# Performance work log

Measured on AMD Instinct MI355X. Metric: run time of the kernel, lower is better.

Reference implementation:

```python
import jax, jax.numpy as jnp
import numpy as np

NUM_LAYERS = 4
HID = 512
EMB = 512
VOCAB = 50000
SOU_LEN = 256
TAR_LEN = 50
BATCH = 8
VEXT = VOCAB + SOU_LEN


def _gru_layer(x, h0, wih, whh, bih, bhh):
    # x: [B,T,in], h0: [B,H]; PyTorch GRU gate order: r, z, n
    def step(h, xt):
        gi = xt @ wih.T + bih
        gh = h @ whh.T + bhh
        ir, iz, inn = jnp.split(gi, 3, axis=-1)
        hr, hz, hn = jnp.split(gh, 3, axis=-1)
        r = jax.nn.sigmoid(ir + hr)
        z = jax.nn.sigmoid(iz + hz)
        n = jnp.tanh(inn + r * hn)
        h_new = (1.0 - z) * n + z * h
        return h_new, h_new
    _, ys = jax.lax.scan(step, h0, jnp.swapaxes(x, 0, 1))
    return jnp.swapaxes(ys, 0, 1)


def _forward(sou, tar, hidden, encoder_outputs, extended_length,
             emb, gru_wih, gru_whh, gru_bih, gru_bhh,
             fc_enc_w, fc_enc_b, fc_dec_w, fc_dec_b, v_w,
             fc_out1_w, fc_out1_b, fc_out2_w, fc_out2_b,
             g1_w, g1_b, g2_w, g2_b, g3_w, g3_b):
    emb = emb.at[0].set(0.0)  # padding_idx=0 (also zeroes its grad)
    tar_emb = emb[tar]  # [B,T,E]
    # pack_padded_sequence: only first `length` steps processed, rest padded with 0
    lengths = jnp.maximum(jnp.sum(tar > 0, axis=-1), 1)
    x = tar_emb
    for l in range(gru_wih.shape[0]):
        x = _gru_layer(x, hidden[l], gru_wih[l], gru_whh[l], gru_bih[l], gru_bhh[l])
    t_idx = jnp.arange(x.shape[1])
    dec_out = jnp.where((t_idx[None, :] < lengths[:, None])[:, :, None], x, 0.0)  # [B,T,H]
    # additive (Bahdanau) attention
    e1 = encoder_outputs @ fc_enc_w.T + fc_enc_b          # [B,S,H]
    e2 = dec_out @ fc_dec_w.T + fc_dec_b                  # [B,T,H]
    energy = jnp.tanh(e1[:, None, :, :] + e2[:, :, None, :])  # [B,T,S,H]
    scores = jnp.einsum('btsh,h->bts', energy, v_w)
    scores = jnp.where((sou == 0)[:, None, :], -jnp.inf, scores)
    atten = jax.nn.softmax(scores, axis=-1)               # [B,T,S]
    weighted = jnp.einsum('bts,bsh->bth', atten, encoder_outputs)
    all_out = jnp.concatenate([weighted, dec_out], axis=-1)  # [B,T,2H]
    mid = all_out @ fc_out2_w.T + fc_out2_b
    logits = mid @ fc_out1_w.T + fc_out1_b                # [B,T,VEXT]
    # extended-vocab mask (vectorized version of the per-batch python loop)
    col = jnp.arange(logits.shape[-1])
    valid = col[None, None, :] < (VOCAB + extended_length)[:, None, None]
    logits = jnp.where(valid, logits, -1e9)
    output_gen = jax.nn.softmax(logits, axis=-1)
    # copy mechanism: scatter-add attention into extended vocab (replaces sparse one-hot bmm)
    def _scatter(att_b, sou_b):
        return jnp.zeros((att_b.shape[0], VEXT), att_b.dtype).at[:, sou_b].add(att_b)
    output_copy = jax.vmap(_scatter)(atten, sou)          # [B,T,VEXT]
    gate = jax.nn.sigmoid(
        jnp.einsum('bth,h->bt', weighted, g1_w) + g1_b[0]
        + jnp.einsum('bth,h->bt', dec_out, g2_w) + g2_b[0]
        + jnp.einsum('bte,e->bt', tar_emb, g3_w) + g3_b[0])[:, :, None]
    output = (1.0 - gate) * output_gen + gate * output_copy
    return output, atten


def setup_inputs() -> dict:
    key = jax.random.key(0)
    ks = jax.random.split(key, 24)
    s = 0.02
    return {
        'sou': jax.random.randint(ks[0], (BATCH, SOU_LEN), 0, VEXT),
        'tar': jax.random.randint(ks[1], (BATCH, TAR_LEN), 0, VEXT),
        'hidden': jax.random.normal(ks[2], (NUM_LAYERS, BATCH, HID), jnp.float32),
        'encoder_outputs': jax.random.normal(ks[3], (BATCH, SOU_LEN, HID), jnp.float32),
        'extended_length': jax.random.randint(ks[4], (BATCH,), 0, SOU_LEN),
        'emb': jax.random.normal(ks[5], (VEXT, EMB), jnp.float32) * s,
        'gru_wih': jax.random.normal(ks[6], (NUM_LAYERS, 3 * HID, EMB), jnp.float32) * s,
        'gru_whh': jax.random.normal(ks[7], (NUM_LAYERS, 3 * HID, HID), jnp.float32) * s,
        'gru_bih': jax.random.normal(ks[8], (NUM_LAYERS, 3 * HID), jnp.float32) * s,
        'gru_bhh': jax.random.normal(ks[9], (NUM_LAYERS, 3 * HID), jnp.float32) * s,
        'fc_enc_w': jax.random.normal(ks[10], (HID, HID), jnp.float32) * s,
        'fc_enc_b': jax.random.normal(ks[11], (HID,), jnp.float32) * s,
        'fc_dec_w': jax.random.normal(ks[12], (HID, HID), jnp.float32) * s,
        'fc_dec_b': jax.random.normal(ks[13], (HID,), jnp.float32) * s,
        'v_w': jax.random.normal(ks[14], (HID,), jnp.float32) * s,
        'fc_out1_w': jax.random.normal(ks[15], (VEXT, HID), jnp.float32) * s,
        'fc_out1_b': jax.random.normal(ks[16], (VEXT,), jnp.float32) * s,
        'fc_out2_w': jax.random.normal(ks[17], (HID, 2 * HID), jnp.float32) * s,
        'fc_out2_b': jax.random.normal(ks[18], (HID,), jnp.float32) * s,
        'g1_w': jax.random.normal(ks[19], (HID,), jnp.float32) * s,
        'g1_b': jnp.zeros((1,), jnp.float32),
        'g2_w': jax.random.normal(ks[20], (HID,), jnp.float32) * s,
        'g2_b': jnp.zeros((1,), jnp.float32),
        'g3_w': jax.random.normal(ks[21], (EMB,), jnp.float32) * s,
        'g3_b': jnp.zeros((1,), jnp.float32),
    }


def reference(sou, tar, hidden, encoder_outputs, extended_length,
              emb, gru_wih, gru_whh, gru_bih, gru_bhh,
              fc_enc_w, fc_enc_b, fc_dec_w, fc_dec_b, v_w,
              fc_out1_w, fc_out1_b, fc_out2_w, fc_out2_b,
              g1_w, g1_b, g2_w, g2_b, g3_w, g3_b):
    return _forward(sou, tar, hidden, encoder_outputs, extended_length,
                    emb, gru_wih, gru_whh, gru_bih, gru_bhh,
                    fc_enc_w, fc_enc_b, fc_dec_w, fc_dec_b, v_w,
                    fc_out1_w, fc_out1_b, fc_out2_w, fc_out2_b,
                    g1_w, g1_b, g2_w, g2_b, g3_w, g3_b)
```

## Files before the change

kernel.cpp:

```cpp
#include <hip/hip_runtime.h>

typedef unsigned short u16;
typedef unsigned int u32;

using bf16x8 = __attribute__((ext_vector_type(8))) short;
using f32x4  = __attribute__((ext_vector_type(4))) float;

#define VOCAB 50000
#define VEXT  50256
#define OUT_AT_OFF 20102400L

__device__ __forceinline__ u16 f2b(float f) {
  u32 x = __float_as_uint(f);
  u32 r = (x + 0x7fffu + ((x >> 16) & 1u)) >> 16;
  return (u16)r;
}

__device__ __forceinline__ u32 sload(const u32* p) {
  return __hip_atomic_load(p, __ATOMIC_RELAXED, __HIP_MEMORY_SCOPE_SYSTEM);
}
__device__ __forceinline__ void sstore(u32* p, u32 v) {
  __hip_atomic_store(p, v, __ATOMIC_RELAXED, __HIP_MEMORY_SCOPE_SYSTEM);
}
__device__ __forceinline__ bf16x8 sload8(const u32* p) {
  union { u32 u[4]; bf16x8 v; } x;
  x.u[0] = sload(p); x.u[1] = sload(p + 1);
  x.u[2] = sload(p + 2); x.u[3] = sload(p + 3);
  return x.v;
}

__global__ void k_conv(const float* __restrict__ src, u16* __restrict__ dst,
                       long realN, long totalN) {
  long i = (long)blockIdx.x * 256 + threadIdx.x;
  if (i >= totalN) return;
  float v = (i < realN) ? src[i] : 0.f;
  dst[i] = f2b(v);
}

__global__ void k_h0b(const float* __restrict__ hidden, u16* __restrict__ h0B) {
  int i = blockIdx.x * 256 + threadIdx.x;
  int l = i >> 13, rem = i & 8191, rr = rem >> 9, k = rem & 511;
  float v = (rr < 8) ? hidden[((long)l * 8 + rr) * 512 + k] : 0.f;
  h0B[i] = f2b(v);
}

__global__ __launch_bounds__(256) void k_prep(const int* __restrict__ tar,
                                              const float* __restrict__ emb,
                                              const float* __restrict__ g3w,
                                              u16* __restrict__ xB0,
                                              float* __restrict__ g3dot) {
  int r = blockIdx.x;
  int tid = threadIdx.x;
  int idx = tar[r];
  __shared__ float red[256];
  float p = 0.f;
  for (int k = tid; k < 512; k += 256) {
    float v = (idx == 0) ? 0.f : emb[(long)idx * 512 + k];
    xB0[(long)r * 512 + k] = f2b(v);
    p += v * g3w[k];
  }
  red[tid] = p; __syncthreads();
  for (int o = 128; o > 0; o >>= 1) { if (tid < o) red[tid] += red[tid + o]; __syncthreads(); }
  if (tid == 0) g3dot[r] = red[0];
}

__global__ void k_lengths(const int* __restrict__ tar, int* __restrict__ lens) {
  int b = threadIdx.x;
  if (b < 8) {
    int c = 0;
    for (int t = 0; t < 50; t++) c += (tar[b * 50 + t] > 0) ? 1 : 0;
    lens[b] = (c > 0) ? c : 1;
  }
}

__global__ __launch_bounds__(256) void k_mask(float* __restrict__ x4f,
                                              const int* __restrict__ lens) {
  int r = blockIdx.x, b = r / 50, t = r % 50;
  if (t >= lens[b])
    for (int k = threadIdx.x; k < 512; k += 256) x4f[(long)r * 512 + k] = 0.f;
}

__device__ __forceinline__ void wait_flags(const u32* f, u32 target) {
  const int lane = threadIdx.x & 63;
  const u32* p = f + (lane & 31) * 16;
  unsigned it = 0;
  while (true) {
    u32 v = sload(p);
    if (__all((int)(v >= target))) break;
    __builtin_amdgcn_s_sleep(2);
    if (++it > (1u << 20)) break;
  }
  asm volatile("" ::: "memory");
}

__global__ __launch_bounds__(128, 1) void k_gru(
    const u16* __restrict__ wihB, const u16* __restrict__ whhB,
    const float* __restrict__ bih, const float* __restrict__ bhh,
    const float* __restrict__ hidden, const u16* __restrict__ h0B,
    u16* __restrict__ xB,
    u32* __restrict__ hX,
    float* __restrict__ x4f,
    u32* __restrict__ flags)
{
  const int wg = blockIdx.x;
  const int l = wg >> 5;
  const int wg32 = wg & 31;
  const int c0 = wg32 << 4;
  const int tid = threadIdx.x;
  const int wv = tid >> 6;
  const int lane = tid & 63;
  const int lrow = lane & 15;
  const int q = lane >> 4;

  __shared__ float giX[2][3][16][16];

  const u16* Wsrc = (wv == 0 ? wihB : whhB) + (long)l * 1536 * 512;

  const int col = c0 + lrow;
  const float bir = bih[l * 1536 + col],         bhr = bhh[l * 1536 + col];
  const float biz = bih[l * 1536 + 512 + col],   bhz = bhh[l * 1536 + 512 + col];
  const float bin_ = bih[l * 1536 + 1024 + col], bhn = bhh[l * 1536 + 1024 + col];

  const u16* xin = xB + (long)l * 16 * 50 * 512;
  u32* xBu = (u32*)xB;
  u32* x4u = (u32*)x4f;

  float hreg[4];
  if (wv == 1) {
#pragma unroll
    for (int rg = 0; rg < 4; rg++) {
      int bb = q * 4 + rg;
      hreg[rg] = (bb < 8) ? hidden[((long)l * 8 + bb) * 512 + col] : 0.f;
    }
  }

  for (int t = 0; t < 50; t++) {
    bf16x8 af[16];
    if (wv == 0) {
      if (l > 0) {
        wait_flags(flags + (l - 1) * 512, (u32)(t + 1));
        const u32* As32 = (const u32*)xin + (long)lrow * 50 * 256 + (long)t * 256;
#pragma unroll
        for (int ks = 0; ks < 16; ks++) af[ks] = sload8(As32 + ks * 16 + q * 4);
      } else {
        const u16* Asrc = xin + (long)lrow * 50 * 512 + (long)t * 512;
#pragma unroll
        for (int ks = 0; ks < 16; ks++) af[ks] = *(const bf16x8*)(Asrc + ks * 32 + q * 8);
      }
    } else {
      if (t > 0) {
        wait_flags(flags + l * 512, (u32)t);
        const u32* Hs = hX + (((long)l * 2 + ((t - 1) & 1)) * 16 + lrow) * 256;
#pragma unroll
        for (int ks = 0; ks < 16; ks++) af[ks] = sload8(Hs + ks * 16 + q * 4);
      } else {
        const u16* Asrc = h0B + ((long)l * 16 + lrow) * 512;
#pragma unroll
        for (int ks = 0; ks < 16; ks++) af[ks] = *(const bf16x8*)(Asrc + ks * 32 + q * 8);
      }
    }

    f32x4 a0 = {0.f, 0.f, 0.f, 0.f}, a1 = {0.f, 0.f, 0.f, 0.f}, a2 = {0.f, 0.f, 0.f, 0.f};
#pragma unroll
    for (int ks = 0; ks < 16; ks++) {
      bf16x8 b0 = *(const bf16x8*)(Wsrc + (long)(0 * 512 + c0 + lrow) * 512 + ks * 32 + q * 8);
      bf16x8 b1 = *(const bf16x8*)(Wsrc + (long)(1 * 512 + c0 + lrow) * 512 + ks * 32 + q * 8);
      bf16x8 b2 = *(const bf16x8*)(Wsrc + (long)(2 * 512 + c0 + lrow) * 512 + ks * 32 + q * 8);
      a0 = __builtin_amdgcn_mfma_f32_16x16x32_bf16(af[ks], b0, a0, 0, 0, 0);
      a1 = __builtin_amdgcn_mfma_f32_16x16x32_bf16(af[ks], b1, a1, 0, 0, 0);
      a2 = __builtin_amdgcn_mfma_f32_16x16x32_bf16(af[ks], b2, a2, 0, 0, 0);
    }

    if (wv == 0) {
#pragma unroll
      for (int rg = 0; rg < 4; rg++) {
        giX[t & 1][0][q * 4 + rg][lrow] = a0[rg];
        giX[t & 1][1][q * 4 + rg][lrow] = a1[rg];
        giX[t & 1][2][q * 4 + rg][lrow] = a2[rg];
      }
    }
    __syncthreads();

    if (wv == 1) {
#pragma unroll
      for (int rg = 0; rg < 4; rg++) {
        int bb = q * 4 + rg;
        float hnew = 0.f;
        u16 hb16 = 0;
        if (bb < 8) {
          float gir = giX[t & 1][0][bb][lrow] + bir;
          float giz = giX[t & 1][1][bb][lrow] + biz;
          float gin = giX[t & 1][2][bb][lrow] + bin_;
          float ghr = a0[rg] + bhr;
          float ghz = a1[rg] + bhz;
          float ghn = a2[rg] + bhn;
          float hprev = hreg[rg];
          float rr = 1.f / (1.f + expf(-(gir + ghr)));
          float zz = 1.f / (1.f + expf(-(giz + ghz)));
          float nn = tanhf(gin + rr * ghn);
          hnew = (1.f - zz) * nn + zz * hprev;
          hreg[rg] = hnew;
          hb16 = f2b(hnew);
        }
        int other = __shfl_xor((int)hb16, 1);
        if (bb < 8) {
          if ((lane & 1) == 0) {
            u32 pr = (u32)hb16 | ((u32)(u16)other << 16);
            long slot = ((long)l * 2 + (t & 1)) * 16 + bb;
            sstore(hX + slot * 256 + (col >> 1), pr);
            if (l < 3)
              sstore(xBu + (((long)(l + 1) * 16 + bb) * 50 + t) * 256 + (col >> 1), pr);
          }
          if (l == 3)
            sstore(x4u + ((long)bb * 50 + t) * 512 + col, __float_as_uint(hnew));
        }
      }
      if (lane == 0)
        __hip_atomic_store(flags + ((long)l * 32 + wg32) * 16, (u32)(t + 1),
                           __ATOMIC_RELEASE, __HIP_MEMORY_SCOPE_SYSTEM);
    }
  }
}

__global__ __launch_bounds__(256, 2) void k_gemm_bf16(
    const u16* __restrict__ A, const u16* __restrict__ Bm,
    const float* __restrict__ bias, float* __restrict__ C,
    int M, int N, int K, int ldc)
{
  __shared__ __align__(16) u16 As[4096];
  __shared__ __align__(16) u16 Bs[4096];
  const int tid = threadIdx.x;
  const int wv = tid >> 6, lane = tid & 63;
  const int wm = wv >> 1, wn = wv & 1;
  const int lrow = lane & 15, q = lane >> 4;
  const int m0 = blockIdx.y * 128, n0 = blockIdx.x * 128;

  f32x4 acc[4][4];
#pragma unroll
  for (int i = 0; i < 4; i++)
#pragma unroll
    for (int j = 0; j < 4; j++) acc[i][j] = {0.f, 0.f, 0.f, 0.f};

  for (int k0 = 0; k0 < K; k0 += 32) {
#pragma unroll
    for (int i = 0; i < 2; i++) {
      int c = i * 256 + tid;
      int row = c >> 2, ko = (c & 3) << 3;
      *(uint4*)(As + c * 8) = *(const uint4*)(A + (long)(m0 + row) * K + k0 + ko);
      *(uint4*)(Bs + c * 8) = *(const uint4*)(Bm + (long)(n0 + row) * K + k0 + ko);
    }
    __syncthreads();
    bf16x8 af[4], bfr[4];
#pragma unroll
    for (int i = 0; i < 4; i++) af[i] = *(const bf16x8*)(As + (wm * 64 + i * 16 + lrow) * 32 + q * 8);
#pragma unroll
    for (int j = 0; j < 4; j++) bfr[j] = *(const bf16x8*)(Bs + (wn * 64 + j * 16 + lrow) * 32 + q * 8);
#pragma unroll
    for (int i = 0; i < 4; i++)
#pragma unroll
      for (int j = 0; j < 4; j++)
        acc[i][j] = __builtin_amdgcn_mfma_f32_16x16x32_bf16(af[i], bfr[j], acc[i][j], 0, 0, 0);
    __syncthreads();
  }

#pragma unroll
  for (int i = 0; i < 4; i++) {
    int rbase = m0 + wm * 64 + i * 16 + q * 4;
#pragma unroll
    for (int j = 0; j < 4; j++) {
      int colg = n0 + wn * 64 + j * 16 + lrow;
      if (colg < N) {
        float bv = bias[colg];
#pragma unroll
        for (int rg = 0; rg < 4; rg++) {
          int rowg = rbase + rg;
          if (rowg < M) C[(long)rowg * ldc + colg] = acc[i][j][rg] + bv;
        }
      }
    }
  }
}

__global__ __launch_bounds__(256) void k_attn(
    const float* __restrict__ e1, const float* __restrict__ e2,
    const float* __restrict__ enc, const float* __restrict__ x4f,
    const int* __restrict__ sou, const float* __restrict__ vw,
    const float* __restrict__ g1w, const float* __restrict__ g1b,
    const float* __restrict__ g2w, const float* __restrict__ g2b,
    const float* __restrict__ g3b, const float* __restrict__ g3dot,
    float* __restrict__ all_out, float* __restrict__ gate,
    float* __restrict__ atten_out)
{
  int r = blockIdx.x;
  int b = r / 50;
  int tid = threadIdx.x;
  __shared__ float e2s[512], decs[512], at[256], red[256];
  for (int k = tid; k < 512; k += 256) {
    e2s[k] = e2[(long)r * 512 + k];
    decs[k] = x4f[(long)r * 512 + k];
  }
  __syncthreads();
  const float* erow = e1 + ((long)b * 256 + tid) * 512;
  float sc = 0.f;
#pragma unroll 4
  for (int h = 0; h < 512; h++) sc += vw[h] * tanhf(erow[h] + e2s[h]);
  if (sou[b * 256 + tid] == 0) sc = -INFINITY;

  red[tid] = sc; __syncthreads();
  for (int o = 128; o > 0; o >>= 1) { if (tid < o) red[tid] = fmaxf(red[tid], red[tid + o]); __syncthreads(); }
  float mx = red[0]; __syncthreads();
  float p = expf(sc - mx);
  red[tid] = p; __syncthreads();
  for (int o = 128; o > 0; o >>= 1) { if (tid < o) red[tid] += red[tid + o]; __syncthreads(); }
  float S = red[0]; __syncthreads();
  float a = p / S;
  at[tid] = a;
  atten_out[(long)r * 256 + tid] = a;
  __syncthreads();

  float pg = 0.f;
  for (int h = tid; h < 512; h += 256) {
    float wsum = 0.f;
    const float* ecol = enc + (long)b * 256 * 512 + h;
    for (int s = 0; s < 256; s++) wsum += at[s] * ecol[(long)s * 512];
    all_out[(long)r * 1024 + h] = wsum;
    all_out[(long)r * 1024 + 512 + h] = decs[h];
    pg += wsum * g1w[h] + decs[h] * g2w[h];
  }
  red[tid] = pg; __syncthreads();
  for (int o = 128; o > 0; o >>= 1) { if (tid < o) red[tid] += red[tid + o]; __syncthreads(); }
  if (tid == 0) {
    float z = red[0] + g1b[0] + g2b[0] + g3dot[r] + g3b[0];
    gate[r] = 1.f / (1.f + expf(-z));
  }
}

__global__ __launch_bounds__(1024) void k_softmax(float* __restrict__ out,
                                                  const float* __restrict__ gate,
                                                  const int* __restrict__ ext) {
  int r = blockIdx.x;
  int b = r / 50;
  int tid = threadIdx.x;
  int nv = VOCAB + ext[b];
  __shared__ float red[1024];
  float* row = out + (long)r * VEXT;
  float m = -INFINITY;
  for (int c = tid; c < nv; c += 1024) m = fmaxf(m, row[c]);
  red[tid] = m; __syncthreads();
  for (int o = 512; o > 0; o >>= 1) { if (tid < o) red[tid] = fmaxf(red[tid], red[tid + o]); __syncthreads(); }
  m = red[0]; __syncthreads();
  float s = 0.f;
  for (int c = tid; c < nv; c += 1024) s += expf(row[c] - m);
  red[tid] = s; __syncthreads();
  for (int o = 512; o > 0; o >>= 1) { if (tid < o) red[tid] += red[tid + o]; __syncthreads(); }
  float inv = (1.f - gate[r]) / red[0];
  for (int c = tid; c < VEXT; c += 1024) {
    float v = (c < nv) ? expf(row[c] - m) * inv : 0.f;
    row[c] = v;
  }
}

__global__ void k_scatter(float* __restrict__ out, const float* __restrict__ atten,
                          const float* __restrict__ gate, const int* __restrict__ sou) {
  int r = blockIdx.x, s = threadIdx.x;
  int b = r / 50;
  float v = gate[r] * atten[(long)r * 256 + s];
  int colv = sou[b * 256 + s];
  atomicAdd(out + (long)r * VEXT + colv, v);
}

extern "C" void kernel_launch(void* const* d_in, const int* in_sizes, int n_in,
                              void* d_out, int out_size, void* d_ws, size_t ws_size,
                              hipStream_t stream) {
  (void)in_sizes; (void)n_in; (void)out_size;
  const int* sou = (const int*)d_in[0];
  const int* tar = (const int*)d_in[1];
  const float* hidden = (const float*)d_in[2];
  const float* enc = (const float*)d_in[3];
  const int* ext = (const int*)d_in[4];
  const float* emb = (const float*)d_in[5];
  const float* wih = (const float*)d_in[6];
  const float* whh = (const float*)d_in[7];
  const float* bih = (const float*)d_in[8];
  const float* bhh = (const float*)d_in[9];
  const float* fc_enc_w = (const float*)d_in[10];
  const float* fc_enc_b = (const float*)d_in[11];
  const float* fc_dec_w = (const float*)d_in[12];
  const float* fc_dec_b = (const float*)d_in[13];
  const float* v_w = (const float*)d_in[14];
  const float* w1 = (const float*)d_in[15];
  const float* b1 = (const float*)d_in[16];
  const float* w2 = (const float*)d_in[17];
  const float* b2 = (const float*)d_in[18];
  const float* g1w = (const float*)d_in[19];
  const float* g1b = (const float*)d_in[20];
  const float* g2w = (const float*)d_in[21];
  const float* g2b = (const float*)d_in[22];
  const float* g3w = (const float*)d_in[23];
  const float* g3b = (const float*)d_in[24];
  float* out = (float*)d_out;

  char* base = (char*)d_ws;
  size_t cur = 0;
  auto alloc = [&](size_t bytes) -> void* {
    void* r = base + cur;
    cur = (cur + bytes + 255) & ~(size_t)255;
    return r;
  };
  u16* wihB = (u16*)alloc(6291456);
  u16* whhB = (u16*)alloc(6291456);
  u16* w1B  = (u16*)alloc(51511296);
  u16* encB = (u16*)alloc(2097152);
  u16* fceB = (u16*)alloc(524288);
  u16* fcdB = (u16*)alloc(524288);
  u16* fo2B = (u16*)alloc(1048576);
  u16* midB = (u16*)alloc(524288);
  u16* decB = (u16*)alloc(524288);
  u16* allB = (u16*)alloc(1048576);
  u16* xB   = (u16*)alloc(3276800);
  u16* h0B  = (u16*)alloc(65536);
  u32* hX   = (u32*)alloc(131072);
  float* x4f = (float*)alloc(819200);
  float* e1 = (float*)alloc(4194304);
  float* e2 = (float*)alloc(819200);
  float* allo = (float*)alloc(1638400);
  float* mid = (float*)alloc(819200);
  float* g3dot = (float*)alloc(1600);
  float* gate = (float*)alloc(1600);
  int* lens = (int*)alloc(32);
  u32* flags = (u32*)alloc(8192);
  if (cur > ws_size) return;

  hipMemsetAsync(flags, 0, 8192, stream);

  k_conv<<<12288, 256, 0, stream>>>(wih, wihB, 3145728L, 3145728L);
  k_conv<<<12288, 256, 0, stream>>>(whh, whhB, 3145728L, 3145728L);
  k_conv<<<100608, 256, 0, stream>>>(w1, w1B, 25731072L, 25755648L);
  k_conv<<<4096, 256, 0, stream>>>(enc, encB, 1048576L, 1048576L);
  k_conv<<<1024, 256, 0, stream>>>(fc_enc_w, fceB, 262144L, 262144L);
  k_conv<<<1024, 256, 0, stream>>>(fc_dec_w, fcdB, 262144L, 262144L);
  k_conv<<<2048, 256, 0, stream>>>(w2, fo2B, 524288L, 524288L);
  k_h0b<<<128, 256, 0, stream>>>(hidden, h0B);
  k_prep<<<400, 256, 0, stream>>>(tar, emb, g3w, xB, g3dot);
  k_lengths<<<1, 64, 0, stream>>>(tar, lens);

  k_gru<<<128, 128, 0, stream>>>(wihB, whhB, bih, bhh, hidden, h0B, xB, hX, x4f, flags);
  k_mask<<<400, 256, 0, stream>>>(x4f, lens);
  k_conv<<<1024, 256, 0, stream>>>(x4f, decB, 204800L, 262144L);

  k_gemm_bf16<<<dim3(4, 16), 256, 0, stream>>>(encB, fceB, fc_enc_b, e1, 2048, 512, 512, 512);
  k_gemm_bf16<<<dim3(4, 4), 256, 0, stream>>>(decB, fcdB, fc_dec_b, e2, 400, 512, 512, 512);
  k_attn<<<400, 256, 0, stream>>>(e1, e2, enc, x4f, sou, v_w, g1w, g1b, g2w, g2b, g3b,
                                  g3dot, allo, gate, out + OUT_AT_OFF);
  k_conv<<<2048, 256, 0, stream>>>(allo, allB, 409600L, 524288L);
  k_gemm_bf16<<<dim3(4, 4), 256, 0, stream>>>(allB, fo2B, b2, mid, 400, 512, 1024, 512);
  k_conv<<<1024, 256, 0, stream>>>(mid, midB, 204800L, 262144L);

  k_gemm_bf16<<<dim3(393, 4), 256, 0, stream>>>(midB, w1B, b1, out, 400, 50256, 512, 50256);
  k_softmax<<<400, 1024, 0, stream>>>(out, gate, ext);
  k_scatter<<<400, 256, 0, stream>>>(out, out + OUT_AT_OFF, gate, sou);
}
```

Baseline: 1.224 ms.

## Replace per-block flag array with atomic counters and widen GRU exchange stores

The GRU cross-workgroup handshake moves from a per-block flag array, polled in parallel by 32 lanes, to a single per-layer counter that each block atomically increments and waiters spin on until it reaches 32*t. Hidden-state exchange stores and loads widen from 32-bit to 64-bit system-scope atomics using an extra shuffle to pack four bf16 values. The layer-3 fp32 output becomes a plain store, and an explicit vmcnt(0) wait replaces release ordering before the relaxed increment. This aims to cut per-step synchronisation latency and memory-op count on the serial 50-step recurrence, at the cost of atomic contention on one address and weaker, hand-managed ordering.

```diff
diff --git a/kernel.cpp b/kernel.cpp
--- a/kernel.cpp
+++ b/kernel.cpp
@@ -2,6 +2,7 @@
 
 typedef unsigned short u16;
 typedef unsigned int u32;
+typedef unsigned long long u64;
 
 using bf16x8 = __attribute__((ext_vector_type(8))) short;
 using f32x4  = __attribute__((ext_vector_type(4))) float;
@@ -16,17 +17,27 @@
   return (u16)r;
 }
 
-__device__ __forceinline__ u32 sload(const u32* p) {
+__device__ __forceinline__ u32 sload32(const u32* p) {
   return __hip_atomic_load(p, __ATOMIC_RELAXED, __HIP_MEMORY_SCOPE_SYSTEM);
 }
-__device__ __forceinline__ void sstore(u32* p, u32 v) {
+__device__ __forceinline__ u64 sload64(const u64* p) {
+  return __hip_atomic_load(p, __ATOMIC_RELAXED, __HIP_MEMORY_SCOPE_SYSTEM);
+}
+__device__ __forceinline__ void sstore64(u64* p, u64 v) {
   __hip_atomic_store(p, v, __ATOMIC_RELAXED, __HIP_MEMORY_SCOPE_SYSTEM);
 }
-__device__ __forceinline__ bf16x8 sload8(const u32* p) {
-  union { u32 u[4]; bf16x8 v; } x;
-  x.u[0] = sload(p); x.u[1] = sload(p + 1);
-  x.u[2] = sload(p + 2); x.u[3] = sload(p + 3);
+__device__ __forceinline__ bf16x8 sload8x(const u64* p) {
+  union { u64 u[2]; bf16x8 v; } x;
+  x.u[0] = sload64(p); x.u[1] = sload64(p + 1);
   return x.v;
+}
+__device__ __forceinline__ void wait_cnt(const u32* c, u32 target) {
+  unsigned it = 0;
+  while (sload32(c) < target) {
+    __builtin_amdgcn_s_sleep(2);
+    if (++it > (1u << 20)) break;
+  }
+  asm volatile("" ::: "memory");
 }
 
 __global__ void k_conv(const float* __restrict__ src, u16* __restrict__ dst,
@@ -80,19 +91,6 @@
     for (int k = threadIdx.x; k < 512; k += 256) x4f[(long)r * 512 + k] = 0.f;
 }
 
-__device__ __forceinline__ void wait_flags(const u32* f, u32 target) {
-  const int lane = threadIdx.x & 63;
-  const u32* p = f + (lane & 31) * 16;
-  unsigned it = 0;
-  while (true) {
-    u32 v = sload(p);
-    if (__all((int)(v >= target))) break;
-    __builtin_amdgcn_s_sleep(2);
-    if (++it > (1u << 20)) break;
-  }
-  asm volatile("" ::: "memory");
-}
-
 __global__ __launch_bounds__(128, 1) void k_gru(
     const u16* __restrict__ wihB, const u16* __restrict__ whhB,
     const float* __restrict__ bih, const float* __restrict__ bhh,
@@ -100,12 +98,11 @@
     u16* __restrict__ xB,
     u32* __restrict__ hX,
     float* __restrict__ x4f,
-    u32* __restrict__ flags)
+    u32* __restrict__ cnt)
 {
   const int wg = blockIdx.x;
   const int l = wg >> 5;
-  const int wg32 = wg & 31;
-  const int c0 = wg32 << 4;
+  const int c0 = (wg & 31) << 4;
   const int tid = threadIdx.x;
   const int wv = tid >> 6;
   const int lane = tid & 63;
@@ -122,8 +119,6 @@
   const float bin_ = bih[l * 1536 + 1024 + col], bhn = bhh[l * 1536 + 1024 + col];
 
   const u16* xin = xB + (long)l * 16 * 50 * 512;
-  u32* xBu = (u32*)xB;
-  u32* x4u = (u32*)x4f;
 
   float hreg[4];
   if (wv == 1) {
@@ -138,10 +133,10 @@
     bf16x8 af[16];
     if (wv == 0) {
       if (l > 0) {
-        wait_flags(flags + (l - 1) * 512, (u32)(t + 1));
-        const u32* As32 = (const u32*)xin + (long)lrow * 50 * 256 + (long)t * 256;
-#pragma unroll
-        for (int ks = 0; ks < 16; ks++) af[ks] = sload8(As32 + ks * 16 + q * 4);
+        wait_cnt(cnt + (l - 1) * 16, 32u * (u32)(t + 1));
+        const u64* A64 = (const u64*)((const u32*)xin + (long)lrow * 50 * 256 + (long)t * 256);
+#pragma unroll
+        for (int ks = 0; ks < 16; ks++) af[ks] = sload8x(A64 + ks * 8 + q * 2);
       } else {
         const u16* Asrc = xin + (long)lrow * 50 * 512 + (long)t * 512;
 #pragma unroll
@@ -149,10 +144,10 @@
       }
     } else {
       if (t > 0) {
-        wait_flags(flags + l * 512, (u32)t);
-        const u32* Hs = hX + (((long)l * 2 + ((t - 1) & 1)) * 16 + lrow) * 256;
-#pragma unroll
-        for (int ks = 0; ks < 16; ks++) af[ks] = sload8(Hs + ks * 16 + q * 4);
+        wait_cnt(cnt + l * 16, 32u * (u32)t);
+        const u64* H64 = (const u64*)(hX + (((long)l * 2 + ((t - 1) & 1)) * 16 + lrow) * 256);
+#pragma unroll
+        for (int ks = 0; ks < 16; ks++) af[ks] = sload8x(H64 + ks * 8 + q * 2);
       } else {
         const u16* Asrc = h0B + ((long)l * 16 + lrow) * 512;
 #pragma unroll
@@ -202,22 +197,22 @@
           hreg[rg] = hnew;
           hb16 = f2b(hnew);
         }
-        int other = __shfl_xor((int)hb16, 1);
+        u32 p32 = (u32)hb16 | ((u32)(u16)__shfl_xor((int)hb16, 1) << 16);
+        u64 p64 = (u64)p32 | ((u64)(u32)__shfl_xor((int)p32, 2) << 32);
         if (bb < 8) {
-          if ((lane & 1) == 0) {
-            u32 pr = (u32)hb16 | ((u32)(u16)other << 16);
+          if ((lrow & 3) == 0) {
             long slot = ((long)l * 2 + (t & 1)) * 16 + bb;
-            sstore(hX + slot * 256 + (col >> 1), pr);
+            sstore64((u64*)hX + slot * 128 + (col >> 2), p64);
             if (l < 3)
-              sstore(xBu + (((long)(l + 1) * 16 + bb) * 50 + t) * 256 + (col >> 1), pr);
+              sstore64((u64*)xB + ((((long)(l + 1) * 16 + bb) * 50 + t) * 128) + (col >> 2), p64);
           }
-          if (l == 3)
-            sstore(x4u + ((long)bb * 50 + t) * 512 + col, __float_as_uint(hnew));
+          if (l == 3) x4f[((long)bb * 50 + t) * 512 + col] = hnew;
         }
       }
+      asm volatile("s_waitcnt vmcnt(0)" ::: "memory");
       if (lane == 0)
-        __hip_atomic_store(flags + ((long)l * 32 + wg32) * 16, (u32)(t + 1),
-                           __ATOMIC_RELEASE, __HIP_MEMORY_SCOPE_SYSTEM);
+        __hip_atomic_fetch_add(cnt + (long)l * 16, 1u,
+                               __ATOMIC_RELAXED, __HIP_MEMORY_SCOPE_SYSTEM);
     }
   }
 }
@@ -428,10 +423,10 @@
   float* g3dot = (float*)alloc(1600);
   float* gate = (float*)alloc(1600);
   int* lens = (int*)alloc(32);
-  u32* flags = (u32*)alloc(8192);
+  u32* cnt = (u32*)alloc(256);
   if (cur > ws_size) return;
 
-  hipMemsetAsync(flags, 0, 8192, stream);
+  hipMemsetAsync(cnt, 0, 256, stream);
 
   k_conv<<<12288, 256, 0, stream>>>(wih, wihB, 3145728L, 3145728L);
   k_conv<<<12288, 256, 0, stream>>>(whh, whhB, 3145728L, 3145728L);
@@ -444,7 +439,7 @@
   k_prep<<<400, 256, 0, stream>>>(tar, emb, g3w, xB, g3dot);
   k_lengths<<<1, 64, 0, stream>>>(tar, lens);
 
-  k_gru<<<128, 128, 0, stream>>>(wihB, whhB, bih, bhh, hidden, h0B, xB, hX, x4f, flags);
+  k_gru<<<128, 128, 0, stream>>>(wihB, whhB, bih, bhh, hidden, h0B, xB, hX, x4f, cnt);
   k_mask<<<400, 256, 0, stream>>>(x4f, lens);
   k_conv<<<1024, 256, 0, stream>>>(x4f, decB, 204800L, 262144L);
 
```

Result: faster. 1.107 ms (-9.6%).
